# Optimization experiments

Hardware: AMD Instinct MI355X
Metric: run time of the kernel (lower is better)

Reference implementation:

```python
import jax, jax.numpy as jnp
import numpy as np

N1, N2, C, G1, G2 = 20000, 80000, 64, 128, 256
K = 27


def _nbr_map(coords, key, G):
    # coords sorted by key = x*G*G + y*G + z; returns [M,27] neighbor idx, -1 if absent
    M = coords.shape[0]
    nbr = np.full((M, K), -1, np.int32)
    k = 0
    for dx in (-1, 0, 1):
        for dy in (-1, 0, 1):
            for dz in (-1, 0, 1):
                nc = coords + np.array([dx, dy, dz])
                valid = np.all((nc >= 0) & (nc < G), axis=1)
                nk = nc[:, 0] * G * G + nc[:, 1] * G + nc[:, 2]
                pos = np.clip(np.searchsorted(key, nk), 0, M - 1)
                hit = valid & (key[pos] == nk)
                nbr[:, k] = np.where(hit, pos, -1)
                k += 1
    return nbr


def setup_inputs() -> dict:
    rng = np.random.default_rng(0)
    # --- parent (curr) level: unique sorted voxels on 128^3 grid ---
    lin = np.sort(rng.choice(G1 ** 3, size=N1, replace=False))
    cc = np.stack([lin // (G1 * G1), (lin // G1) % G1, lin % G1], axis=1)
    # occupancy codes with exactly 4 set bits -> exactly 4 children per parent
    bits4 = np.argsort(rng.random((N1, 8)), axis=1)[:, :4]  # [N1,4]
    curr_occ = (1 << bits4).sum(axis=1).astype(np.int32)[:, None]
    # --- FCG expansion: child coords = parent*2 + octant offset ---
    off = np.stack([(bits4 >> 2) & 1, (bits4 >> 1) & 1, bits4 & 1], axis=-1)
    child = (cc[:, None, :] * 2 + off).reshape(-1, 3)
    parent_idx = np.repeat(np.arange(N1, dtype=np.int32), 4)
    ckey = child[:, 0] * G2 * G2 + child[:, 1] * G2 + child[:, 2]
    o = np.argsort(ckey)  # op.sort_CF
    child, parent_idx, ckey = child[o], parent_idx[o], ckey[o]
    next_octant = ((child[:, 0] % 2) * 4 + (child[:, 1] % 2) * 2 + (child[:, 2] % 2)).astype(np.int32)
    next_occ = rng.integers(0, 256, size=(N2, 1)).astype(np.int32)
    nbr_curr = _nbr_map(cc, lin, G1)
    nbr_next = _nbr_map(child, ckey, G2)

    key = jax.random.key(0)
    ks = jax.random.split(key, 16)
    f32 = jnp.float32
    inp = {
        'prior_emb': jax.random.normal(ks[0], (256, C), f32),
        'target_emb8': jax.random.normal(ks[1], (8, C), f32),
        'Wp': jax.random.normal(ks[2], (5, K, C, C), f32) * 0.03,
        'Wt': jax.random.normal(ks[3], (5, K, C, C), f32) * 0.03,
        'W0a': jax.random.normal(ks[4], (C, C), f32) * 0.1,
        'b0a': jnp.zeros((C,), f32),
        'W0b': jax.random.normal(ks[5], (C, 16), f32) * 0.1,
        'b0b': jnp.zeros((16,), f32),
        'W1a': jax.random.normal(ks[6], (C, C), f32) * 0.1,
        'b1a': jnp.zeros((C,), f32),
        'W1b': jax.random.normal(ks[7], (C, 16), f32) * 0.1,
        'b1b': jnp.zeros((16,), f32),
        's1_emb': jax.random.normal(ks[8], (16, C), f32),
        'curr_occ': jnp.asarray(curr_occ),
        'next_occ': jnp.asarray(next_occ),
        'next_octant': jnp.asarray(next_octant),
        'parent_idx': jnp.asarray(parent_idx),
        'nbr_curr': jnp.asarray(nbr_curr),
        'nbr_next': jnp.asarray(nbr_next),
        'n_points': 640000,
    }
    return inp


def _sp_conv(feats, nbr, W):
    # 3x3x3 sparse conv via kernel map: out[i] = sum_k feats[nbr[i,k]] @ W[k]
    out = jnp.zeros((feats.shape[0], W.shape[-1]), feats.dtype)
    for k in range(K):
        idx = nbr[:, k]
        g = jnp.where((idx >= 0)[:, None], feats[jnp.clip(idx, 0, None)], 0.0)
        out = out + g @ W[k]
    return out


def _resnet(feats, nbr, Wa, Wb):
    h = jax.nn.relu(_sp_conv(feats, nbr, Wa))
    h = _sp_conv(h, nbr, Wb)
    return jax.nn.relu(feats + h)


def reference(prior_emb, target_emb8, Wp, Wt, W0a, b0a, W0b, b0b, W1a, b1a, W1b, b1b, s1_emb,
              curr_occ, next_occ, next_octant, parent_idx, nbr_curr, nbr_next, n_points):
    # prior branch on parent level
    f = prior_emb[curr_occ[:, 0]]                              # [N1,C]
    f = jax.nn.relu(_sp_conv(f, nbr_curr, Wp[0]))
    f = _resnet(f, nbr_curr, Wp[1], Wp[2])
    f = _resnet(f, nbr_curr, Wp[3], Wp[4])
    # FCG: broadcast parent feats to children, add octant (target) embedding
    g = f[parent_idx] + target_emb8[next_octant]               # [N2,C]
    g = jax.nn.relu(_sp_conv(g, nbr_next, Wt[0]))
    g = _resnet(g, nbr_next, Wt[1], Wt[2])
    g = _resnet(g, nbr_next, Wt[3], Wt[4])
    # bit-prediction heads
    lower = jnp.remainder(next_occ, 16)                        # [N2,1]
    upper = next_occ // 16                                     # [N2,1]
    lp = jax.nn.softmax(jax.nn.relu(g @ W0a + b0a) @ W0b + b0b, axis=-1)
    h1 = g + s1_emb[lower[:, 0]]
    up = jax.nn.softmax(jax.nn.relu(h1 @ W1a + b1a) @ W1b + b1b, axis=-1)
    lp_gt = jnp.take_along_axis(lp, lower, axis=1)
    up_gt = jnp.take_along_axis(up, upper, axis=1)
    eps = 1e-10
    bits = jnp.sum(jnp.clip(-jnp.log2(lp_gt + eps), 0.0, 50.0))
    bits = bits + jnp.sum(jnp.clip(-jnp.log2(up_gt + eps), 0.0, 50.0))
    return bits / n_points
```

## Files before the change

kernel.cpp:

```cpp
#include <hip/hip_runtime.h>

#define NP1 20000
#define NP2 80000
#define KN  27

typedef unsigned short ushort;
typedef unsigned int   uint;
typedef __attribute__((ext_vector_type(8))) short short8v;
typedef __attribute__((ext_vector_type(4))) float f32x4;

__device__ __forceinline__ ushort f2bf(float x) {
    union { float f; uint u; } v; v.f = x;
    uint r = v.u + 0x7fffu + ((v.u >> 16) & 1u);
    return (ushort)(r >> 16);
}
__device__ __forceinline__ float bf2f(ushort s) {
    union { uint u; float f; } v; v.u = ((uint)s) << 16;
    return v.f;
}
__device__ __forceinline__ void gload_lds16(const void* g, void* l) {
    __builtin_amdgcn_global_load_lds(
        (const __attribute__((address_space(1))) unsigned int*)g,
        (__attribute__((address_space(3))) unsigned int*)l, 16, 0, 0);
}
__device__ __forceinline__ int xcd_swz(int b, int nb) {
    int q = nb >> 3, r = nb & 7;
    int x = b & 7, p = b >> 3;
    return (x < r) ? x * (q + 1) + p : r * (q + 1) + (x - r) * q + p;
}

__global__ __launch_bounds__(256) void prep_wT_tile_k(
    const float* __restrict__ Wp, const float* __restrict__ Wt,
    ushort* __restrict__ dstp, ushort* __restrict__ dstt)
{
    __shared__ float sT[64 * 65];
    int b = blockIdx.x;
    const float* W = (b < 135) ? Wp : Wt;
    ushort* dst    = (b < 135) ? dstp : dstt;
    int k = (b < 135) ? b : b - 135;
    const float* src = W + (size_t)k * 4096;
    int t = threadIdx.x;
    #pragma unroll
    for (int p = 0; p < 16; ++p) {
        int i = t + p * 256;
        sT[(i >> 6) * 65 + (i & 63)] = src[i];
    }
    __syncthreads();
    ushort* d = dst + (size_t)k * 4096;
    #pragma unroll
    for (int p = 0; p < 16; ++p) {
        int o = t + p * 256;
        int c = o >> 6, jj = o & 63;
        int j = (((jj >> 3) ^ (c & 7)) << 3) | (jj & 7);
        d[o] = f2bf(sT[j * 65 + c]);
    }
}

__global__ __launch_bounds__(256) void prep_small_k(
    const float* __restrict__ W0a, const float* __restrict__ W1a,
    const float* __restrict__ W0b, const float* __restrict__ W1b,
    const float* __restrict__ s1,
    ushort* __restrict__ W0aT, ushort* __restrict__ W1aT,
    ushort* __restrict__ W0bT, ushort* __restrict__ W1bT,
    ushort* __restrict__ s1bT)
{
    int b = blockIdx.x, t = threadIdx.x;
    if (b < 32) {
        const float* W = (b < 16) ? W0a : W1a;
        ushort* dst    = (b < 16) ? W0aT : W1aT;
        int i = (b & 15) * 256 + t;
        int c = i >> 6, jj = i & 63;
        int j = (((jj >> 3) ^ (c & 7)) << 3) | (jj & 7);
        dst[i] = f2bf(W[j * 64 + c]);
    } else if (b < 40) {
        const float* W = (b < 36) ? W0b : W1b;
        ushort* dst    = (b < 36) ? W0bT : W1bT;
        int i = (b - ((b < 36) ? 32 : 36)) * 256 + t;
        int c = i >> 6, jj = i & 63;
        int j = (((jj >> 3) ^ (c & 7)) << 3) | (jj & 7);
        dst[i] = f2bf(W[j * 16 + c]);
    } else {
        int i = (b - 40) * 256 + t;
        int e = i >> 6, jj = i & 63;
        int j = (((jj >> 3) ^ (e & 7)) << 3) | (jj & 7);
        s1bT[i] = f2bf(s1[e * 64 + j]);
    }
}

__global__ __launch_bounds__(256) void gather_curr_k(
    const float* __restrict__ prior_emb, const int* __restrict__ curr_occ,
    ushort* __restrict__ out)
{
    int i = blockIdx.x * 256 + threadIdx.x;
    if (i >= NP1 * 32) return;
    int row = i >> 5, cp = (i & 31) * 2;
    const float* src = prior_emb + (size_t)curr_occ[row] * 64 + cp;
    uint pk = (uint)f2bf(src[0]) | ((uint)f2bf(src[1]) << 16);
    *(uint*)((char*)out + (size_t)row * 128 + cp * 2) = pk;
}

__global__ __launch_bounds__(256) void gather_next_k(
    const ushort* __restrict__ f, const int* __restrict__ parent_idx,
    const int* __restrict__ next_oct, const float* __restrict__ temb8,
    ushort* __restrict__ out)
{
    int i = blockIdx.x * 256 + threadIdx.x;
    if (i >= NP2 * 32) return;
    int row = i >> 5, cp = (i & 31) * 2;
    const ushort* fs = f + (size_t)parent_idx[row] * 64 + cp;
    const float* ts = temb8 + (size_t)next_oct[row] * 64 + cp;
    float v0 = bf2f(fs[0]) + ts[0];
    float v1 = bf2f(fs[1]) + ts[1];
    uint pk = (uint)f2bf(v0) | ((uint)f2bf(v1) << 16);
    *(uint*)((char*)out + (size_t)row * 128 + cp * 2) = pk;
}

template<int NW>
__global__ __launch_bounds__(NW * 64) void spconv_reg_k(
    const ushort* __restrict__ feats, const int* __restrict__ nbr,
    const ushort* __restrict__ Wsw, const ushort* __restrict__ res,
    ushort* __restrict__ out, const ushort* __restrict__ zpage, int nblocks)
{
    constexpr int ROWS   = NW * 16;
    constexpr int WLOADS = 8192 / (NW * 64 * 16);

    __shared__ __align__(16) char sW[2 * 8192];

    const int t = threadIdx.x;
    const int w = t >> 6, l = t & 63;
    const int wg = xcd_swz(blockIdx.x, nblocks);
    const int row0 = wg * ROWS;
    const int lr = l & 15, lhi = l >> 4;
    const int ch0 = lhi ^ (lr & 7);
    const int ch1 = (4 + lhi) ^ (lr & 7);

    const int* nbrow = nbr + (size_t)(row0 + w * 16 + lr) * KN;

    f32x4 acc[4];
    #pragma unroll
    for (int b = 0; b < 4; ++b) acc[b] = (f32x4)0.0f;

    short8v aC0, aC1, aN0, aN1;
    int idxA, idxB;

    #define LOADA(IDX, CHOFF) \
        (*(const short8v*)(((IDX) >= 0 ? (const char*)feats + (size_t)(IDX) * 128 \
                                       : (const char*)zpage) + ((CHOFF) + lhi) * 16))

    {
        int id0 = nbrow[0];
        aC0 = LOADA(id0, 0);
        aC1 = LOADA(id0, 4);
        idxA = nbrow[1];
        const char* wsrc = (const char*)Wsw;
        #pragma unroll
        for (int i = 0; i < WLOADS; ++i) {
            int off = (w * WLOADS + i) * 1024;
            gload_lds16(wsrc + off + l * 16, sW + off);
        }
    }

    for (int k = 0; k < KN; ++k) {
        char* cur = sW + (k & 1) * 8192;
        char* nxt = sW + ((k + 1) & 1) * 8192;

        __syncthreads();

        if (k < KN - 1) {
            const char* wsrc = (const char*)Wsw + (size_t)(k + 1) * 8192;
            #pragma unroll
            for (int i = 0; i < WLOADS; ++i) {
                int off = (w * WLOADS + i) * 1024;
                gload_lds16(wsrc + off + l * 16, nxt + off);
            }
            aN0 = LOADA(idxA, 0);
            aN1 = LOADA(idxA, 4);
        }
        if (k < KN - 2) idxB = nbrow[k + 2];

        __builtin_amdgcn_s_setprio(1);
        {
            short8v b0[4];
            #pragma unroll
            for (int nb = 0; nb < 4; ++nb)
                b0[nb] = *(const short8v*)(cur + (nb * 16 + lr) * 128 + ch0 * 16);
            #pragma unroll
            for (int nb = 0; nb < 4; ++nb)
                acc[nb] = __builtin_amdgcn_mfma_f32_16x16x32_bf16(aC0, b0[nb], acc[nb], 0, 0, 0);
            short8v b1[4];
            #pragma unroll
            for (int nb = 0; nb < 4; ++nb)
                b1[nb] = *(const short8v*)(cur + (nb * 16 + lr) * 128 + ch1 * 16);
            #pragma unroll
            for (int nb = 0; nb < 4; ++nb)
                acc[nb] = __builtin_amdgcn_mfma_f32_16x16x32_bf16(aC1, b1[nb], acc[nb], 0, 0, 0);
        }
        __builtin_amdgcn_s_setprio(0);

        aC0 = aN0; aC1 = aN1; idxA = idxB;
    }
    #undef LOADA

    #pragma unroll
    for (int nb = 0; nb < 4; ++nb) {
        #pragma unroll
        for (int r = 0; r < 4; ++r) {
            int rg = row0 + w * 16 + lhi * 4 + r;
            int c = nb * 16 + lr;
            float v = acc[nb][r];
            if (res != nullptr) v += bf2f(res[(size_t)rg * 64 + c]);
            v = fmaxf(v, 0.0f);
            float o = __shfl_xor(v, 1);
            if (!(l & 1)) {
                uint pk = (uint)f2bf(v) | ((uint)f2bf(o) << 16);
                *(uint*)((char*)out + (size_t)rg * 128 + (c << 1)) = pk;
            }
        }
    }
}

__global__ __launch_bounds__(256) void head_mfma_k(
    const ushort* __restrict__ G, const int* __restrict__ next_occ,
    const ushort* __restrict__ Wsmall,
    const float* __restrict__ b0a, const float* __restrict__ b1a,
    const float* __restrict__ b0b, const float* __restrict__ b1b,
    const int* __restrict__ n_points, float* __restrict__ outp)
{
    __shared__ __align__(16) char sm[32768 + 22528 + 640 + 8704 + 32];
    char* sG = sm;
    char* sH = sm + 16384;
    char* sWs = sm + 32768;
    float* sBf = (float*)(sm + 32768 + 22528);
    float* sL  = (float*)(sm + 32768 + 22528 + 640);
    float* sRed = (float*)(sm + 32768 + 22528 + 640 + 8704);

    const int t = threadIdx.x;
    const int w = t >> 6, l = t & 63;
    const int row0 = blockIdx.x * 128;
    const int lr = l & 15, lhi = l >> 4;
    const int wr0 = w * 32;
    const int myrow = wr0 + (l & 31);
    const int occ_l = next_occ[row0 + myrow];

    #pragma unroll
    for (int i = 0; i < 4; ++i) {
        int rt = w * 32 + i * 8 + (l >> 3);
        int row = row0 + rt;
        gload_lds16((const char*)G + (size_t)row * 128 + (((l & 7) ^ (rt & 7)) << 4),
                    sG + (w * 32 + i * 8) * 128);
    }
    for (int i = w; i < 22; i += 4)
        gload_lds16((const char*)Wsmall + i * 1024 + l * 16, sWs + i * 1024);
    if (t < 64)                 sBf[t] = b0a[t];
    else if (t < 128)           sBf[t] = b1a[t - 64];
    else if (t < 144)           sBf[128 + (t - 128)] = b0b[t - 128];
    else if (t < 160)           sBf[144 + (t - 144)] = b1b[t - 144];
    __syncthreads();

    float bacc = 0.0f;
    f32x4 lg[2];

    {
        f32x4 acc[2][4];
        #pragma unroll
        for (int a = 0; a < 2; ++a)
            #pragma unroll
            for (int b = 0; b < 4; ++b) acc[a][b] = (f32x4)0.0f;
        #pragma unroll
        for (int j0 = 0; j0 < 2; ++j0) {
            short8v a[2], b[4];
            #pragma unroll
            for (int mb = 0; mb < 2; ++mb) {
                int r = wr0 + mb * 16 + lr;
                int ch = (j0 * 4 + lhi) ^ (r & 7);
                a[mb] = *(const short8v*)(sG + r * 128 + ch * 16);
            }
            #pragma unroll
            for (int nb = 0; nb < 4; ++nb) {
                int c = nb * 16 + lr;
                int ch = (j0 * 4 + lhi) ^ (c & 7);
                b[nb] = *(const short8v*)(sWs + c * 128 + ch * 16);
            }
            #pragma unroll
            for (int mb = 0; mb < 2; ++mb)
                #pragma unroll
                for (int nb = 0; nb < 4; ++nb)
                    acc[mb][nb] = __builtin_amdgcn_mfma_f32_16x16x32_bf16(
                        a[mb], b[nb], acc[mb][nb], 0, 0, 0);
        }
        #pragma unroll
        for (int mb = 0; mb < 2; ++mb)
            #pragma unroll
            for (int nb = 0; nb < 4; ++nb) {
                float bias = sBf[nb * 16 + lr];
                #pragma unroll
                for (int r = 0; r < 4; ++r) {
                    int row = wr0 + mb * 16 + lhi * 4 + r;
                    int j = nb * 16 + lr;
                    float v = fmaxf(acc[mb][nb][r] + bias, 0.0f);
                    float o = __shfl_xor(v, 1);
                    if (!(l & 1)) {
                        uint pk = (uint)f2bf(v) | ((uint)f2bf(o) << 16);
                        *(uint*)(sH + row * 128 + (((j >> 3) ^ (row & 7)) << 4)
                                 + (j & 7) * 2) = pk;
                    }
                }
            }
        lg[0] = (f32x4)0.0f; lg[1] = (f32x4)0.0f;
        #pragma unroll
        for (int j0 = 0; j0 < 2; ++j0) {
            short8v a[2], b;
            #pragma unroll
            for (int mb = 0; mb < 2; ++mb) {
                int r = wr0 + mb * 16 + lr;
                int ch = (j0 * 4 + lhi) ^ (r & 7);
                a[mb] = *(const short8v*)(sH + r * 128 + ch * 16);
            }
            {
                int c = lr;
                int ch = (j0 * 4 + lhi) ^ (c & 7);
                b = *(const short8v*)(sWs + 16384 + c * 128 + ch * 16);
            }
            #pragma unroll
            for (int mb = 0; mb < 2; ++mb)
                lg[mb] = __builtin_amdgcn_mfma_f32_16x16x32_bf16(a[mb], b, lg[mb], 0, 0, 0);
        }
        #pragma unroll
        for (int mb = 0; mb < 2; ++mb)
            #pragma unroll
            for (int r = 0; r < 4; ++r)
                sL[(wr0 + mb * 16 + lhi * 4 + r) * 17 + lr] = lg[mb][r] + sBf[128 + lr];
        asm volatile("s_waitcnt lgkmcnt(0)" ::: "memory");
        __builtin_amdgcn_sched_barrier(0);
        {
            int tgt = occ_l & 15;
            float lv[16], mx = -1e30f;
            #pragma unroll
            for (int c = 0; c < 16; ++c) {
                lv[c] = sL[myrow * 17 + c];
                mx = fmaxf(mx, lv[c]);
            }
            float ssum = 0.0f, lt = lv[0];
            #pragma unroll
            for (int c = 0; c < 16; ++c) {
                ssum += __expf(lv[c] - mx);
                lt = (c == tgt) ? lv[c] : lt;
            }
            float p = __expf(lt - mx) / ssum;
            float bits = fminf(fmaxf(-log2f(p + 1e-10f), 0.0f), 50.0f);
            if (l < 32) bacc += bits;
        }
    }

    {
        f32x4 acc1[2][4];
        #pragma unroll
        for (int a = 0; a < 2; ++a)
            #pragma unroll
            for (int b = 0; b < 4; ++b) acc1[a][b] = (f32x4)0.0f;
        #pragma unroll
        for (int j0 = 0; j0 < 2; ++j0) {
            short8v a[2], b[4];
            #pragma unroll
            for (int mb = 0; mb < 2; ++mb) {
                int rloc = wr0 + mb * 16 + lr;
                int low = next_occ[row0 + rloc] & 15;
                int ch = (j0 * 4 + lhi) ^ (rloc & 7);
                short8v g8 = *(const short8v*)(sG + rloc * 128 + ch * 16);
                int che = (j0 * 4 + lhi) ^ (low & 7);
                short8v e8 = *(const short8v*)(sWs + 20480 + low * 128 + che * 16);
                #pragma unroll
                for (int e = 0; e < 8; ++e) {
                    float f = bf2f((ushort)g8[e]) + bf2f((ushort)e8[e]);
                    a[mb][e] = (short)f2bf(f);
                }
            }
            #pragma unroll
            for (int nb = 0; nb < 4; ++nb) {
                int c = nb * 16 + lr;
                int ch = (j0 * 4 + lhi) ^ (c & 7);
                b[nb] = *(const short8v*)(sWs + 8192 + c * 128 + ch * 16);
            }
            #pragma unroll
            for (int mb = 0; mb < 2; ++mb)
                #pragma unroll
                for (int nb = 0; nb < 4; ++nb)
                    acc1[mb][nb] = __builtin_amdgcn_mfma_f32_16x16x32_bf16(
                        a[mb], b[nb], acc1[mb][nb], 0, 0, 0);
        }
        #pragma unroll
        for (int mb = 0; mb < 2; ++mb)
            #pragma unroll
            for (int nb = 0; nb < 4; ++nb) {
                float bias = sBf[64 + nb * 16 + lr];
                #pragma unroll
                for (int r = 0; r < 4; ++r) {
                    int row = wr0 + mb * 16 + lhi * 4 + r;
                    int j = nb * 16 + lr;
                    float v = fmaxf(acc1[mb][nb][r] + bias, 0.0f);
                    float o = __shfl_xor(v, 1);
                    if (!(l & 1)) {
                        uint pk = (uint)f2bf(v) | ((uint)f2bf(o) << 16);
                        *(uint*)(sH + row * 128 + (((j >> 3) ^ (row & 7)) << 4)
                                 + (j & 7) * 2) = pk;
                    }
                }
            }
        lg[0] = (f32x4)0.0f; lg[1] = (f32x4)0.0f;
        #pragma unroll
        for (int j0 = 0; j0 < 2; ++j0) {
            short8v a[2], b;
            #pragma unroll
            for (int mb = 0; mb < 2; ++mb) {
                int r = wr0 + mb * 16 + lr;
                int ch = (j0 * 4 + lhi) ^ (r & 7);
                a[mb] = *(const short8v*)(sH + r * 128 + ch * 16);
            }
            {
                int c = lr;
                int ch = (j0 * 4 + lhi) ^ (c & 7);
                b = *(const short8v*)(sWs + 18432 + c * 128 + ch * 16);
            }
            #pragma unroll
            for (int mb = 0; mb < 2; ++mb)
                lg[mb] = __builtin_amdgcn_mfma_f32_16x16x32_bf16(a[mb], b, lg[mb], 0, 0, 0);
        }
        #pragma unroll
        for (int mb = 0; mb < 2; ++mb)
            #pragma unroll
            for (int r = 0; r < 4; ++r)
                sL[(wr0 + mb * 16 + lhi * 4 + r) * 17 + lr] = lg[mb][r] + sBf[144 + lr];
        asm volatile("s_waitcnt lgkmcnt(0)" ::: "memory");
        __builtin_amdgcn_sched_barrier(0);
        {
            int tgt = occ_l >> 4;
            float lv[16], mx = -1e30f;
            #pragma unroll
            for (int c = 0; c < 16; ++c) {
                lv[c] = sL[myrow * 17 + c];
                mx = fmaxf(mx, lv[c]);
            }
            float ssum = 0.0f, lt = lv[0];
            #pragma unroll
            for (int c = 0; c < 16; ++c) {
                ssum += __expf(lv[c] - mx);
                lt = (c == tgt) ? lv[c] : lt;
            }
            float p = __expf(lt - mx) / ssum;
            float bits = fminf(fmaxf(-log2f(p + 1e-10f), 0.0f), 50.0f);
            if (l < 32) bacc += bits;
        }
    }

    #pragma unroll
    for (int s = 1; s < 64; s <<= 1) bacc += __shfl_xor(bacc, s);
    if (l == 0) sRed[w] = bacc;
    __syncthreads();
    if (t == 0)
        atomicAdd(outp, (sRed[0] + sRed[1] + sRed[2] + sRed[3]) / (float)(*n_points));
}

extern "C" void kernel_launch(void* const* d_in, const int* in_sizes, int n_in,
                              void* d_out, int out_size, void* d_ws, size_t ws_size,
                              hipStream_t stream)
{
    const float* prior_emb = (const float*)d_in[0];
    const float* temb8     = (const float*)d_in[1];
    const float* Wp        = (const float*)d_in[2];
    const float* Wt        = (const float*)d_in[3];
    const float* W0a       = (const float*)d_in[4];
    const float* b0a       = (const float*)d_in[5];
    const float* W0b       = (const float*)d_in[6];
    const float* b0b       = (const float*)d_in[7];
    const float* W1a       = (const float*)d_in[8];
    const float* b1a       = (const float*)d_in[9];
    const float* W1b       = (const float*)d_in[10];
    const float* b1b       = (const float*)d_in[11];
    const float* s1_emb    = (const float*)d_in[12];
    const int*   curr_occ  = (const int*)d_in[13];
    const int*   next_occ  = (const int*)d_in[14];
    const int*   next_oct  = (const int*)d_in[15];
    const int*   parent    = (const int*)d_in[16];
    const int*   nbr_curr  = (const int*)d_in[17];
    const int*   nbr_next  = (const int*)d_in[18];
    const int*   n_points  = (const int*)d_in[19];
    float* out = (float*)d_out;

    char* wsb = (char*)d_ws;
    ushort* zpage = (ushort*)wsb;
    size_t off = 256;
    ushort* WpT = (ushort*)(wsb + off); off += (size_t)135 * 4096 * 2;
    ushort* WtT = (ushort*)(wsb + off); off += (size_t)135 * 4096 * 2;
    ushort* Wsmall = (ushort*)(wsb + off);
    ushort* W0aT = Wsmall;
    ushort* W1aT = Wsmall + 4096;
    ushort* W0bT = Wsmall + 8192;
    ushort* W1bT = Wsmall + 9216;
    ushort* s1bT = Wsmall + 10240;
    off += 11264 * 2;
    off = (off + 255) & ~(size_t)255;
    ushort* fA = (ushort*)(wsb + off); off += (size_t)NP1 * 64 * 2;
    ushort* fB = (ushort*)(wsb + off); off += (size_t)NP1 * 64 * 2;
    ushort* fC = (ushort*)(wsb + off); off += (size_t)NP1 * 64 * 2;
    ushort* gA = (ushort*)(wsb + off); off += (size_t)NP2 * 64 * 2;
    ushort* gB = (ushort*)(wsb + off); off += (size_t)NP2 * 64 * 2;
    ushort* gC = (ushort*)(wsb + off); off += (size_t)NP2 * 64 * 2;

    hipMemsetAsync(d_out, 0, sizeof(float), stream);
    hipMemsetAsync(zpage, 0, 256, stream);

    prep_wT_tile_k<<<270, 256, 0, stream>>>(Wp, Wt, WpT, WtT);
    prep_small_k<<<44, 256, 0, stream>>>(W0a, W1a, W0b, W1b, s1_emb,
                                         W0aT, W1aT, W0bT, W1bT, s1bT);

    gather_curr_k<<<(NP1 * 32 + 255) / 256, 256, 0, stream>>>(prior_emb, curr_occ, fA);

    const size_t WT = (size_t)KN * 4096;
    spconv_reg_k<2><<<625, 128, 0, stream>>>(fA, nbr_curr, WpT + 0 * WT, nullptr, fB, zpage, 625);
    spconv_reg_k<2><<<625, 128, 0, stream>>>(fB, nbr_curr, WpT + 1 * WT, nullptr, fC, zpage, 625);
    spconv_reg_k<2><<<625, 128, 0, stream>>>(fC, nbr_curr, WpT + 2 * WT, fB,      fA, zpage, 625);
    spconv_reg_k<2><<<625, 128, 0, stream>>>(fA, nbr_curr, WpT + 3 * WT, nullptr, fC, zpage, 625);
    spconv_reg_k<2><<<625, 128, 0, stream>>>(fC, nbr_curr, WpT + 4 * WT, fA,      fB, zpage, 625);

    gather_next_k<<<(NP2 * 32 + 255) / 256, 256, 0, stream>>>(fB, parent, next_oct, temb8, gA);

    spconv_reg_k<8><<<625, 512, 0, stream>>>(gA, nbr_next, WtT + 0 * WT, nullptr, gB, zpage, 625);
    spconv_reg_k<8><<<625, 512, 0, stream>>>(gB, nbr_next, WtT + 1 * WT, nullptr, gC, zpage, 625);
    spconv_reg_k<8><<<625, 512, 0, stream>>>(gC, nbr_next, WtT + 2 * WT, gB,      gA, zpage, 625);
    spconv_reg_k<8><<<625, 512, 0, stream>>>(gA, nbr_next, WtT + 3 * WT, nullptr, gC, zpage, 625);
    spconv_reg_k<8><<<625, 512, 0, stream>>>(gC, nbr_next, WtT + 4 * WT, gA,      gB, zpage, 625);

    head_mfma_k<<<625, 256, 0, stream>>>(gB, next_occ, Wsmall,
                                         b0a, b1a, b0b, b1b, n_points, out);
}
```

Baseline: 261.0 us.

## Split spconv output columns across waves and restructure head kernel per-wave

The spconv kernel gains a column-group parameter, so the parent-level convs run 4 waves per block with each pair of waves splitting the 64 output channels. That raises waves per block and cuts per-wave accumulators without changing the block count. The head kernel is rewritten to use 8 waves, each handling 16 rows. Each wave loads its A fragments straight from global memory into registers instead of staging G in LDS, and keeps private LDS scratch for the hidden and logit tiles. This trades some A-fragment reuse and duplicated neighbor-index and feature loads for more parallelism and less LDS traffic.

```diff
diff --git a/kernel.cpp b/kernel.cpp
--- a/kernel.cpp
+++ b/kernel.cpp
@@ -115,13 +115,14 @@
     *(uint*)((char*)out + (size_t)row * 128 + cp * 2) = pk;
 }
 
-template<int NW>
+template<int NW, int CG>
 __global__ __launch_bounds__(NW * 64) void spconv_reg_k(
     const ushort* __restrict__ feats, const int* __restrict__ nbr,
     const ushort* __restrict__ Wsw, const ushort* __restrict__ res,
     ushort* __restrict__ out, const ushort* __restrict__ zpage, int nblocks)
 {
-    constexpr int ROWS   = NW * 16;
+    constexpr int ROWS   = (NW / CG) * 16;
+    constexpr int NB     = 4 / CG;
     constexpr int WLOADS = 8192 / (NW * 64 * 16);
 
     __shared__ __align__(16) char sW[2 * 8192];
@@ -131,14 +132,16 @@
     const int wg = xcd_swz(blockIdx.x, nblocks);
     const int row0 = wg * ROWS;
     const int lr = l & 15, lhi = l >> 4;
+    const int colbase = (w % CG) * (NB * 16);
+    const int rw = w / CG;
     const int ch0 = lhi ^ (lr & 7);
     const int ch1 = (4 + lhi) ^ (lr & 7);
 
-    const int* nbrow = nbr + (size_t)(row0 + w * 16 + lr) * KN;
-
-    f32x4 acc[4];
+    const int* nbrow = nbr + (size_t)(row0 + rw * 16 + lr) * KN;
+
+    f32x4 acc[NB];
     #pragma unroll
-    for (int b = 0; b < 4; ++b) acc[b] = (f32x4)0.0f;
+    for (int b = 0; b < NB; ++b) acc[b] = (f32x4)0.0f;
 
     short8v aC0, aC1, aN0, aN1;
     int idxA, idxB;
@@ -180,19 +183,19 @@
 
         __builtin_amdgcn_s_setprio(1);
         {
-            short8v b0[4];
-            #pragma unroll
-            for (int nb = 0; nb < 4; ++nb)
-                b0[nb] = *(const short8v*)(cur + (nb * 16 + lr) * 128 + ch0 * 16);
-            #pragma unroll
-            for (int nb = 0; nb < 4; ++nb)
+            short8v b0[NB];
+            #pragma unroll
+            for (int nb = 0; nb < NB; ++nb)
+                b0[nb] = *(const short8v*)(cur + (colbase + nb * 16 + lr) * 128 + ch0 * 16);
+            #pragma unroll
+            for (int nb = 0; nb < NB; ++nb)
                 acc[nb] = __builtin_amdgcn_mfma_f32_16x16x32_bf16(aC0, b0[nb], acc[nb], 0, 0, 0);
-            short8v b1[4];
-            #pragma unroll
-            for (int nb = 0; nb < 4; ++nb)
-                b1[nb] = *(const short8v*)(cur + (nb * 16 + lr) * 128 + ch1 * 16);
-            #pragma unroll
-            for (int nb = 0; nb < 4; ++nb)
+            short8v b1[NB];
+            #pragma unroll
+            for (int nb = 0; nb < NB; ++nb)
+                b1[nb] = *(const short8v*)(cur + (colbase + nb * 16 + lr) * 128 + ch1 * 16);
+            #pragma unroll
+            for (int nb = 0; nb < NB; ++nb)
                 acc[nb] = __builtin_amdgcn_mfma_f32_16x16x32_bf16(aC1, b1[nb], acc[nb], 0, 0, 0);
         }
         __builtin_amdgcn_s_setprio(0);
@@ -202,11 +205,11 @@
     #undef LOADA
 
     #pragma unroll
-    for (int nb = 0; nb < 4; ++nb) {
+    for (int nb = 0; nb < NB; ++nb) {
         #pragma unroll
         for (int r = 0; r < 4; ++r) {
-            int rg = row0 + w * 16 + lhi * 4 + r;
-            int c = nb * 16 + lr;
+            int rg = row0 + rw * 16 + lhi * 4 + r;
+            int c = colbase + nb * 16 + lr;
             float v = acc[nb][r];
             if (res != nullptr) v += bf2f(res[(size_t)rg * 64 + c]);
             v = fmaxf(v, 0.0f);
@@ -219,117 +222,87 @@
     }
 }
 
-__global__ __launch_bounds__(256) void head_mfma_k(
+__global__ __launch_bounds__(512) void head_v2_k(
     const ushort* __restrict__ G, const int* __restrict__ next_occ,
     const ushort* __restrict__ Wsmall,
     const float* __restrict__ b0a, const float* __restrict__ b1a,
     const float* __restrict__ b0b, const float* __restrict__ b1b,
     const int* __restrict__ n_points, float* __restrict__ outp)
 {
-    __shared__ __align__(16) char sm[32768 + 22528 + 640 + 8704 + 32];
-    char* sG = sm;
-    char* sH = sm + 16384;
-    char* sWs = sm + 32768;
-    float* sBf = (float*)(sm + 32768 + 22528);
-    float* sL  = (float*)(sm + 32768 + 22528 + 640);
-    float* sRed = (float*)(sm + 32768 + 22528 + 640 + 8704);
+    __shared__ __align__(16) char sm[48288];
+    char*  sWs = sm;
+    char*  sHb = sm + 22528;
+    float* sLb = (float*)(sm + 38912);
+    float* sBf = (float*)(sm + 47616);
+    float* sRed = (float*)(sm + 48256);
 
     const int t = threadIdx.x;
     const int w = t >> 6, l = t & 63;
     const int row0 = blockIdx.x * 128;
     const int lr = l & 15, lhi = l >> 4;
-    const int wr0 = w * 32;
-    const int myrow = wr0 + (l & 31);
-    const int occ_l = next_occ[row0 + myrow];
-
-    #pragma unroll
-    for (int i = 0; i < 4; ++i) {
-        int rt = w * 32 + i * 8 + (l >> 3);
-        int row = row0 + rt;
-        gload_lds16((const char*)G + (size_t)row * 128 + (((l & 7) ^ (rt & 7)) << 4),
-                    sG + (w * 32 + i * 8) * 128);
-    }
-    for (int i = w; i < 22; i += 4)
+    char*  sH = sHb + w * 2048;
+    float* sL = sLb + w * 272;
+
+    const int myrow = row0 + w * 16 + lr;
+    const int occ_l = next_occ[myrow];
+
+    short8v aG0 = *(const short8v*)((const char*)G + (size_t)myrow * 128 + lhi * 16);
+    short8v aG1 = *(const short8v*)((const char*)G + (size_t)myrow * 128 + (4 + lhi) * 16);
+
+    for (int i = w; i < 22; i += 8)
         gload_lds16((const char*)Wsmall + i * 1024 + l * 16, sWs + i * 1024);
-    if (t < 64)                 sBf[t] = b0a[t];
-    else if (t < 128)           sBf[t] = b1a[t - 64];
-    else if (t < 144)           sBf[128 + (t - 128)] = b0b[t - 128];
-    else if (t < 160)           sBf[144 + (t - 144)] = b1b[t - 144];
+    if (t < 64)       sBf[t] = b0a[t];
+    else if (t < 128) sBf[t] = b1a[t - 64];
+    else if (t < 144) sBf[128 + (t - 128)] = b0b[t - 128];
+    else if (t < 160) sBf[144 + (t - 144)] = b1b[t - 144];
     __syncthreads();
 
     float bacc = 0.0f;
-    f32x4 lg[2];
 
     {
-        f32x4 acc[2][4];
-        #pragma unroll
-        for (int a = 0; a < 2; ++a)
-            #pragma unroll
-            for (int b = 0; b < 4; ++b) acc[a][b] = (f32x4)0.0f;
+        f32x4 a0[4];
+        #pragma unroll
+        for (int b = 0; b < 4; ++b) a0[b] = (f32x4)0.0f;
         #pragma unroll
         for (int j0 = 0; j0 < 2; ++j0) {
-            short8v a[2], b[4];
-            #pragma unroll
-            for (int mb = 0; mb < 2; ++mb) {
-                int r = wr0 + mb * 16 + lr;
-                int ch = (j0 * 4 + lhi) ^ (r & 7);
-                a[mb] = *(const short8v*)(sG + r * 128 + ch * 16);
-            }
+            short8v a = j0 ? aG1 : aG0;
             #pragma unroll
             for (int nb = 0; nb < 4; ++nb) {
                 int c = nb * 16 + lr;
                 int ch = (j0 * 4 + lhi) ^ (c & 7);
-                b[nb] = *(const short8v*)(sWs + c * 128 + ch * 16);
-            }
-            #pragma unroll
-            for (int mb = 0; mb < 2; ++mb)
-                #pragma unroll
-                for (int nb = 0; nb < 4; ++nb)
-                    acc[mb][nb] = __builtin_amdgcn_mfma_f32_16x16x32_bf16(
-                        a[mb], b[nb], acc[mb][nb], 0, 0, 0);
-        }
-        #pragma unroll
-        for (int mb = 0; mb < 2; ++mb)
-            #pragma unroll
-            for (int nb = 0; nb < 4; ++nb) {
-                float bias = sBf[nb * 16 + lr];
-                #pragma unroll
-                for (int r = 0; r < 4; ++r) {
-                    int row = wr0 + mb * 16 + lhi * 4 + r;
-                    int j = nb * 16 + lr;
-                    float v = fmaxf(acc[mb][nb][r] + bias, 0.0f);
-                    float o = __shfl_xor(v, 1);
-                    if (!(l & 1)) {
-                        uint pk = (uint)f2bf(v) | ((uint)f2bf(o) << 16);
-                        *(uint*)(sH + row * 128 + (((j >> 3) ^ (row & 7)) << 4)
-                                 + (j & 7) * 2) = pk;
-                    }
+                short8v b = *(const short8v*)(sWs + c * 128 + ch * 16);
+                a0[nb] = __builtin_amdgcn_mfma_f32_16x16x32_bf16(a, b, a0[nb], 0, 0, 0);
+            }
+        }
+        #pragma unroll
+        for (int nb = 0; nb < 4; ++nb) {
+            float bias = sBf[nb * 16 + lr];
+            #pragma unroll
+            for (int r = 0; r < 4; ++r) {
+                int row = lhi * 4 + r;
+                int j = nb * 16 + lr;
+                float v = fmaxf(a0[nb][r] + bias, 0.0f);
+                float o = __shfl_xor(v, 1);
+                if (!(l & 1)) {
+                    uint pk = (uint)f2bf(v) | ((uint)f2bf(o) << 16);
+                    *(uint*)(sH + row * 128 + (((j >> 3) ^ (row & 7)) << 4)
+                             + (j & 7) * 2) = pk;
                 }
             }
-        lg[0] = (f32x4)0.0f; lg[1] = (f32x4)0.0f;
+        }
+        asm volatile("s_waitcnt lgkmcnt(0)" ::: "memory");
+        __builtin_amdgcn_sched_barrier(0);
+        f32x4 lg = (f32x4)0.0f;
         #pragma unroll
         for (int j0 = 0; j0 < 2; ++j0) {
-            short8v a[2], b;
-            #pragma unroll
-            for (int mb = 0; mb < 2; ++mb) {
-                int r = wr0 + mb * 16 + lr;
-                int ch = (j0 * 4 + lhi) ^ (r & 7);
-                a[mb] = *(const short8v*)(sH + r * 128 + ch * 16);
-            }
-            {
-                int c = lr;
-                int ch = (j0 * 4 + lhi) ^ (c & 7);
-                b = *(const short8v*)(sWs + 16384 + c * 128 + ch * 16);
-            }
-            #pragma unroll
-            for (int mb = 0; mb < 2; ++mb)
-                lg[mb] = __builtin_amdgcn_mfma_f32_16x16x32_bf16(a[mb], b, lg[mb], 0, 0, 0);
-        }
-        #pragma unroll
-        for (int mb = 0; mb < 2; ++mb)
-            #pragma unroll
-            for (int r = 0; r < 4; ++r)
-                sL[(wr0 + mb * 16 + lhi * 4 + r) * 17 + lr] = lg[mb][r] + sBf[128 + lr];
+            int ch = (j0 * 4 + lhi) ^ (lr & 7);
+            short8v a = *(const short8v*)(sH + lr * 128 + ch * 16);
+            short8v b = *(const short8v*)(sWs + 16384 + lr * 128 + ch * 16);
+            lg = __builtin_amdgcn_mfma_f32_16x16x32_bf16(a, b, lg, 0, 0, 0);
+        }
+        #pragma unroll
+        for (int r = 0; r < 4; ++r)
+            sL[(lhi * 4 + r) * 17 + lr] = lg[r] + sBf[128 + lr];
         asm volatile("s_waitcnt lgkmcnt(0)" ::: "memory");
         __builtin_amdgcn_sched_barrier(0);
         {
@@ -337,7 +310,7 @@
             float lv[16], mx = -1e30f;
             #pragma unroll
             for (int c = 0; c < 16; ++c) {
-                lv[c] = sL[myrow * 17 + c];
+                lv[c] = sL[lr * 17 + c];
                 mx = fmaxf(mx, lv[c]);
             }
             float ssum = 0.0f, lt = lv[0];
@@ -348,88 +321,63 @@
             }
             float p = __expf(lt - mx) / ssum;
             float bits = fminf(fmaxf(-log2f(p + 1e-10f), 0.0f), 50.0f);
-            if (l < 32) bacc += bits;
+            if (l < 16) bacc += bits;
         }
     }
 
     {
-        f32x4 acc1[2][4];
-        #pragma unroll
-        for (int a = 0; a < 2; ++a)
-            #pragma unroll
-            for (int b = 0; b < 4; ++b) acc1[a][b] = (f32x4)0.0f;
+        f32x4 a1[4];
+        #pragma unroll
+        for (int b = 0; b < 4; ++b) a1[b] = (f32x4)0.0f;
+        int low_l = occ_l & 15;
         #pragma unroll
         for (int j0 = 0; j0 < 2; ++j0) {
-            short8v a[2], b[4];
-            #pragma unroll
-            for (int mb = 0; mb < 2; ++mb) {
-                int rloc = wr0 + mb * 16 + lr;
-                int low = next_occ[row0 + rloc] & 15;
-                int ch = (j0 * 4 + lhi) ^ (rloc & 7);
-                short8v g8 = *(const short8v*)(sG + rloc * 128 + ch * 16);
-                int che = (j0 * 4 + lhi) ^ (low & 7);
-                short8v e8 = *(const short8v*)(sWs + 20480 + low * 128 + che * 16);
-                #pragma unroll
-                for (int e = 0; e < 8; ++e) {
-                    float f = bf2f((ushort)g8[e]) + bf2f((ushort)e8[e]);
-                    a[mb][e] = (short)f2bf(f);
-                }
+            short8v g8 = j0 ? aG1 : aG0;
+            int che = (j0 * 4 + lhi) ^ (low_l & 7);
+            short8v e8 = *(const short8v*)(sWs + 20480 + low_l * 128 + che * 16);
+            short8v a;
+            #pragma unroll
+            for (int e = 0; e < 8; ++e) {
+                float f = bf2f((ushort)g8[e]) + bf2f((ushort)e8[e]);
+                a[e] = (short)f2bf(f);
             }
             #pragma unroll
             for (int nb = 0; nb < 4; ++nb) {
                 int c = nb * 16 + lr;
                 int ch = (j0 * 4 + lhi) ^ (c & 7);
-                b[nb] = *(const short8v*)(sWs + 8192 + c * 128 + ch * 16);
-            }
-            #pragma unroll
-            for (int mb = 0; mb < 2; ++mb)
-                #pragma unroll
-                for (int nb = 0; nb < 4; ++nb)
-                    acc1[mb][nb] = __builtin_amdgcn_mfma_f32_16x16x32_bf16(
-                        a[mb], b[nb], acc1[mb][nb], 0, 0, 0);
-        }
-        #pragma unroll
-        for (int mb = 0; mb < 2; ++mb)
-            #pragma unroll
-            for (int nb = 0; nb < 4; ++nb) {
-                float bias = sBf[64 + nb * 16 + lr];
-                #pragma unroll
-                for (int r = 0; r < 4; ++r) {
-                    int row = wr0 + mb * 16 + lhi * 4 + r;
-                    int j = nb * 16 + lr;
-                    float v = fmaxf(acc1[mb][nb][r] + bias, 0.0f);
-                    float o = __shfl_xor(v, 1);
-                    if (!(l & 1)) {
-                        uint pk = (uint)f2bf(v) | ((uint)f2bf(o) << 16);
-                        *(uint*)(sH + row * 128 + (((j >> 3) ^ (row & 7)) << 4)
-                                 + (j & 7) * 2) = pk;
-                    }
+                short8v b = *(const short8v*)(sWs + 8192 + c * 128 + ch * 16);
+                a1[nb] = __builtin_amdgcn_mfma_f32_16x16x32_bf16(a, b, a1[nb], 0, 0, 0);
+            }
+        }
+        #pragma unroll
+        for (int nb = 0; nb < 4; ++nb) {
+            float bias = sBf[64 + nb * 16 + lr];
+            #pragma unroll
+            for (int r = 0; r < 4; ++r) {
+                int row = lhi * 4 + r;
+                int j = nb * 16 + lr;
+                float v = fmaxf(a1[nb][r] + bias, 0.0f);
+                float o = __shfl_xor(v, 1);
+                if (!(l & 1)) {
+                    uint pk = (uint)f2bf(v) | ((uint)f2bf(o) << 16);
+                    *(uint*)(sH + row * 128 + (((j >> 3) ^ (row & 7)) << 4)
+                             + (j & 7) * 2) = pk;
                 }
             }
-        lg[0] = (f32x4)0.0f; lg[1] = (f32x4)0.0f;
+        }
+        asm volatile("s_waitcnt lgkmcnt(0)" ::: "memory");
+        __builtin_amdgcn_sched_barrier(0);
+        f32x4 lg = (f32x4)0.0f;
         #pragma unroll
         for (int j0 = 0; j0 < 2; ++j0) {
-            short8v a[2], b;
-            #pragma unroll
-            for (int mb = 0; mb < 2; ++mb) {
-                int r = wr0 + mb * 16 + lr;
-                int ch = (j0 * 4 + lhi) ^ (r & 7);
-                a[mb] = *(const short8v*)(sH + r * 128 + ch * 16);
-            }
-            {
-                int c = lr;
-                int ch = (j0 * 4 + lhi) ^ (c & 7);
-                b = *(const short8v*)(sWs + 18432 + c * 128 + ch * 16);
-            }
-            #pragma unroll
-            for (int mb = 0; mb < 2; ++mb)
-                lg[mb] = __builtin_amdgcn_mfma_f32_16x16x32_bf16(a[mb], b, lg[mb], 0, 0, 0);
-        }
-        #pragma unroll
-        for (int mb = 0; mb < 2; ++mb)
-            #pragma unroll
-            for (int r = 0; r < 4; ++r)
-                sL[(wr0 + mb * 16 + lhi * 4 + r) * 17 + lr] = lg[mb][r] + sBf[144 + lr];
+            int ch = (j0 * 4 + lhi) ^ (lr & 7);
+            short8v a = *(const short8v*)(sH + lr * 128 + ch * 16);
+            short8v b = *(const short8v*)(sWs + 18432 + lr * 128 + ch * 16);
+            lg = __builtin_amdgcn_mfma_f32_16x16x32_bf16(a, b, lg, 0, 0, 0);
+        }
+        #pragma unroll
+        for (int r = 0; r < 4; ++r)
+            sL[(lhi * 4 + r) * 17 + lr] = lg[r] + sBf[144 + lr];
         asm volatile("s_waitcnt lgkmcnt(0)" ::: "memory");
         __builtin_amdgcn_sched_barrier(0);
         {
@@ -437,7 +385,7 @@
             float lv[16], mx = -1e30f;
             #pragma unroll
             for (int c = 0; c < 16; ++c) {
-                lv[c] = sL[myrow * 17 + c];
+                lv[c] = sL[lr * 17 + c];
                 mx = fmaxf(mx, lv[c]);
             }
             float ssum = 0.0f, lt = lv[0];
@@ -448,7 +396,7 @@
             }
             float p = __expf(lt - mx) / ssum;
             float bits = fminf(fmaxf(-log2f(p + 1e-10f), 0.0f), 50.0f);
-            if (l < 32) bacc += bits;
+            if (l < 16) bacc += bits;
         }
     }
 
@@ -456,8 +404,12 @@
     for (int s = 1; s < 64; s <<= 1) bacc += __shfl_xor(bacc, s);
     if (l == 0) sRed[w] = bacc;
     __syncthreads();
-    if (t == 0)
-        atomicAdd(outp, (sRed[0] + sRed[1] + sRed[2] + sRed[3]) / (float)(*n_points));
+    if (t == 0) {
+        float s = 0.0f;
+        #pragma unroll
+        for (int i = 0; i < 8; ++i) s += sRed[i];
+        atomicAdd(outp, s / (float)(*n_points));
+    }
 }
 
 extern "C" void kernel_launch(void* const* d_in, const int* in_sizes, int n_in,
@@ -516,20 +468,20 @@
     gather_curr_k<<<(NP1 * 32 + 255) / 256, 256, 0, stream>>>(prior_emb, curr_occ, fA);
 
     const size_t WT = (size_t)KN * 4096;
-    spconv_reg_k<2><<<625, 128, 0, stream>>>(fA, nbr_curr, WpT + 0 * WT, nullptr, fB, zpage, 625);
-    spconv_reg_k<2><<<625, 128, 0, stream>>>(fB, nbr_curr, WpT + 1 * WT, nullptr, fC, zpage, 625);
-    spconv_reg_k<2><<<625, 128, 0, stream>>>(fC, nbr_curr, WpT + 2 * WT, fB,      fA, zpage, 625);
-    spconv_reg_k<2><<<625, 128, 0, stream>>>(fA, nbr_curr, WpT + 3 * WT, nullptr, fC, zpage, 625);
-    spconv_reg_k<2><<<625, 128, 0, stream>>>(fC, nbr_curr, WpT + 4 * WT, fA,      fB, zpage, 625);
+    spconv_reg_k<4,2><<<625, 256, 0, stream>>>(fA, nbr_curr, WpT + 0 * WT, nullptr, fB, zpage, 625);
+    spconv_reg_k<4,2><<<625, 256, 0, stream>>>(fB, nbr_curr, WpT + 1 * WT, nullptr, fC, zpage, 625);
+    spconv_reg_k<4,2><<<625, 256, 0, stream>>>(fC, nbr_curr, WpT + 2 * WT, fB,      fA, zpage, 625);
+    spconv_reg_k<4,2><<<625, 256, 0, stream>>>(fA, nbr_curr, WpT + 3 * WT, nullptr, fC, zpage, 625);
+    spconv_reg_k<4,2><<<625, 256, 0, stream>>>(fC, nbr_curr, WpT + 4 * WT, fA,      fB, zpage, 625);
 
     gather_next_k<<<(NP2 * 32 + 255) / 256, 256, 0, stream>>>(fB, parent, next_oct, temb8, gA);
 
-    spconv_reg_k<8><<<625, 512, 0, stream>>>(gA, nbr_next, WtT + 0 * WT, nullptr, gB, zpage, 625);
-    spconv_reg_k<8><<<625, 512, 0, stream>>>(gB, nbr_next, WtT + 1 * WT, nullptr, gC, zpage, 625);
-    spconv_reg_k<8><<<625, 512, 0, stream>>>(gC, nbr_next, WtT + 2 * WT, gB,      gA, zpage, 625);
-    spconv_reg_k<8><<<625, 512, 0, stream>>>(gA, nbr_next, WtT + 3 * WT, nullptr, gC, zpage, 625);
-    spconv_reg_k<8><<<625, 512, 0, stream>>>(gC, nbr_next, WtT + 4 * WT, gA,      gB, zpage, 625);
-
-    head_mfma_k<<<625, 256, 0, stream>>>(gB, next_occ, Wsmall,
-                                         b0a, b1a, b0b, b1b, n_points, out);
-}
+    spconv_reg_k<8,1><<<625, 512, 0, stream>>>(gA, nbr_next, WtT + 0 * WT, nullptr, gB, zpage, 625);
+    spconv_reg_k<8,1><<<625, 512, 0, stream>>>(gB, nbr_next, WtT + 1 * WT, nullptr, gC, zpage, 625);
+    spconv_reg_k<8,1><<<625, 512, 0, stream>>>(gC, nbr_next, WtT + 2 * WT, gB,      gA, zpage, 625);
+    spconv_reg_k<8,1><<<625, 512, 0, stream>>>(gA, nbr_next, WtT + 3 * WT, nullptr, gC, zpage, 625);
+    spconv_reg_k<8,1><<<625, 512, 0, stream>>>(gC, nbr_next, WtT + 4 * WT, gA,      gB, zpage, 625);
+
+    head_v2_k<<<625, 512, 0, stream>>>(gB, next_occ, Wsmall,
+                                       b0a, b1a, b0b, b1b, n_points, out);
+}
```

Measured after the change: 258.8 us, median of 3. Within noise of the previous version (-0.8%).
